# Performance work log

Measured on AMD Instinct MI355X. Metric: run time of the kernel, lower is better.

The kernel has to match this reference:

```python
import jax, jax.numpy as jnp
import numpy as np

N = 50000   # nodes
E = 640000  # edges (before self-loops)
D = 128     # in_channels = hidden_channels = out_channels
EPS_BN = 1e-5


def _gat(x, src, dst, W, a_src, a_dst, b, heads, concat):
    """PyG-style GATConv (self-loops already appended to src/dst)."""
    n = x.shape[0]
    C = W.shape[1] // heads
    xp = (x @ W).reshape(n, heads, C)                      # [N,H,C]
    asrc = jnp.sum(xp * a_src, -1)                          # [N,H]
    adst = jnp.sum(xp * a_dst, -1)                          # [N,H]
    e = jax.nn.leaky_relu(asrc[src] + adst[dst], 0.2)       # [Etot,H]
    m = jax.ops.segment_max(e, dst, num_segments=n)
    ex = jnp.exp(e - m[dst])
    s = jax.ops.segment_sum(ex, dst, num_segments=n)
    alpha = ex / (s[dst] + 1e-16)                           # segment softmax
    out = jax.ops.segment_sum(xp[src] * alpha[..., None], dst, num_segments=n)
    out = out.reshape(n, heads * C) if concat else out.mean(1)
    return out + b


def _gru(x, h, Wih, Whh, bih, bhh):
    gi = x @ Wih + bih
    gh = h @ Whh + bhh
    ir, iz, inn = jnp.split(gi, 3, -1)
    hr, hz, hn = jnp.split(gh, 3, -1)
    r = jax.nn.sigmoid(ir + hr)
    z = jax.nn.sigmoid(iz + hz)
    nn_ = jnp.tanh(inn + r * hn)
    return (1.0 - z) * nn_ + z * h


def setup_inputs() -> dict:
    key = jax.random.key(0)
    ks = jax.random.split(key, 32)
    f32 = jnp.float32
    p = lambda k, shape, s=0.1: jax.random.normal(k, shape, f32) * s
    inp = {
        "node_features": jax.random.normal(ks[0], (N, D), f32),
        "edge_index": jax.random.randint(ks[1], (2, E), 0, N),
        "x_prev1": jax.random.normal(ks[2], (N, D), f32),
        "x_prev2": jax.random.normal(ks[3], (N, D), f32),
        "ts": jax.random.uniform(ks[4], (N, 1), f32),
        # TimeEncode params
        "basis_freq": jnp.asarray(1.0 / 10 ** np.linspace(0, 9, D), f32),
        "phase": jnp.zeros((D,), f32),
        # MergeLayer: Linear(2D -> D)
        "merge_W": p(ks[5], (2 * D, D)),
        "merge_b": p(ks[6], (D,)),
        # layer1 GATConv(D -> D, heads=1, concat)
        "gat1_W": p(ks[7], (D, D)),
        "gat1_asrc": p(ks[8], (1, D)),
        "gat1_adst": p(ks[9], (1, D)),
        "gat1_b": p(ks[10], (D,)),
        # layer1 GRUCell(D, D)
        "gru1_Wih": p(ks[11], (D, 3 * D)),
        "gru1_Whh": p(ks[12], (D, 3 * D)),
        "gru1_bih": p(ks[13], (3 * D,)),
        "gru1_bhh": p(ks[14], (3 * D,)),
        # layer2 GATConv(D -> D, heads=1, concat=False)
        "gat2_W": p(ks[15], (D, D)),
        "gat2_asrc": p(ks[16], (1, D)),
        "gat2_adst": p(ks[17], (1, D)),
        "gat2_b": p(ks[18], (D,)),
        # layer2 GRUCell(D, D)
        "gru2_Wih": p(ks[19], (D, 3 * D)),
        "gru2_Whh": p(ks[20], (D, 3 * D)),
        "gru2_bih": p(ks[21], (3 * D,)),
        "gru2_bhh": p(ks[22], (3 * D,)),
        # skip connection Linear(D -> D)
        "skip_W": p(ks[23], (D, D)),
        "skip_b": p(ks[24], (D,)),
    }
    return inp


def reference(node_features, edge_index, x_prev1, x_prev2, ts,
              basis_freq, phase, merge_W, merge_b,
              gat1_W, gat1_asrc, gat1_adst, gat1_b,
              gru1_Wih, gru1_Whh, gru1_bih, gru1_bhh,
              gat2_W, gat2_asrc, gat2_adst, gat2_b,
              gru2_Wih, gru2_Whh, gru2_bih, gru2_bhh,
              skip_W, skip_b):
    n = node_features.shape[0]
    loop = jnp.arange(n)
    src = jnp.concatenate([edge_index[0], loop])  # add self-loops (PyG default)
    dst = jnp.concatenate([edge_index[1], loop])

    # TimeEncode: cos(ts * freq + phase) -> [N, D]
    t_embed = jnp.cos(ts * basis_freq[None, :] + phase[None, :])
    # MergeLayer
    x = jnp.concatenate([node_features, t_embed], -1) @ merge_W + merge_b

    # layer1: GAT + GRU, relu
    h1c = _gat(x, src, dst, gat1_W, gat1_asrc, gat1_adst, gat1_b, 1, True)
    H1 = jax.nn.relu(_gru(h1c, x_prev1, gru1_Wih, gru1_Whh, gru1_bih, gru1_bhh))

    # layer2: GAT + GRU + skip + fresh BatchNorm1d (training stats, identity affine)
    h2c = _gat(H1, src, dst, gat2_W, gat2_asrc, gat2_adst, gat2_b, 1, False)
    H2 = _gru(h2c, x_prev2, gru2_Wih, gru2_Whh, gru2_bih, gru2_bhh)
    H2 = H2 + (x @ skip_W + skip_b)
    mu = H2.mean(0)
    var = H2.var(0)
    H2 = (H2 - mu) / jnp.sqrt(var + EPS_BN)
    return (H1, H2)
```

## Files before the change

### kernel.cpp

```cpp
#include <hip/hip_runtime.h>
#include <math.h>

#define D 128
#define D3 384

typedef __attribute__((ext_vector_type(8))) short bf16x8;
typedef __attribute__((ext_vector_type(4))) float f32x4;
typedef __attribute__((ext_vector_type(4))) unsigned int u32x4;

__device__ __forceinline__ float fsigmoid(float x){
  return __builtin_amdgcn_rcpf(1.0f + __expf(-x));
}
__device__ __forceinline__ float ftanh(float x){
  float e = __expf(2.0f * x);
  return 1.0f - 2.0f * __builtin_amdgcn_rcpf(e + 1.0f);
}

__device__ __forceinline__ unsigned short f2bf(float f){
  unsigned u = __float_as_uint(f);
  return (unsigned short)((u + 0x7FFFu + ((u >> 16) & 1u)) >> 16);
}

__device__ __forceinline__ int slot16(int c, int row){ return (c + 2 * (row & 7)) & 15; }
__device__ __forceinline__ int slot32(int c, int row){ return (c + 2 * (row & 7)) & 31; }

__global__ __launch_bounds__(256) void k_init0(int* __restrict__ cnt, float* __restrict__ bns, int n){
  int idx = blockIdx.x * 256 + threadIdx.x;
  if (idx < n) cnt[idx] = 0;
  if (idx < 2 * D) bns[idx] = 0.0f;
}

__global__ __launch_bounds__(256) void k_wpackall(
    const float* __restrict__ mergeW, const float* __restrict__ g0, const float* __restrict__ g1,
    const float* __restrict__ sk, const float* __restrict__ ih0, const float* __restrict__ hh0,
    const float* __restrict__ ih1, const float* __restrict__ hh1,
    unsigned short* __restrict__ Pm, unsigned short* __restrict__ Pg0, unsigned short* __restrict__ Pg1,
    unsigned short* __restrict__ Psk, unsigned short* __restrict__ Pu0, unsigned short* __restrict__ Pu1){
  int idx = blockIdx.x * 256 + threadIdx.x;
  if (idx < 32768){
    int i = idx;
    int j = i & 7, l15 = (i >> 3) & 15, lg = (i >> 7) & 3, nf = (i >> 9) & 1, kk = (i >> 10) & 7, w = (i >> 13) & 3;
    int col = w * 32 + nf * 16 + l15, k = (kk * 4 + lg) * 8 + j;
    Pm[i] = f2bf(mergeW[k * 128 + col]);
  } else if (idx < 81920){
    int seg = (idx - 32768) >> 14;
    int i = (idx - 32768) & 16383;
    const float* W = seg == 0 ? g0 : (seg == 1 ? g1 : sk);
    unsigned short* P = seg == 0 ? Pg0 : (seg == 1 ? Pg1 : Psk);
    int j = i & 7, l15 = (i >> 3) & 15, lg = (i >> 7) & 3, nf = (i >> 9) & 1, kk = (i >> 10) & 3, w = (i >> 12) & 3;
    int col = w * 32 + nf * 16 + l15, k = (kk * 4 + lg) * 8 + j;
    P[i] = f2bf(W[k * 128 + col]);
  } else if (idx < 278528){
    int seg = (idx - 81920) / 98304;
    int i = (idx - 81920) % 98304;
    const float* Wih = seg ? ih1 : ih0;
    const float* Whh = seg ? hh1 : hh0;
    unsigned short* P = seg ? Pu1 : Pu0;
    int j = i & 7, l15 = (i >> 3) & 15, lg = (i >> 7) & 3;
    int r9 = i >> 9; int t = r9 % 6; int r = r9 / 6; int kk = r & 3, w = r >> 2;
    int col = (t >> 1) * 128 + w * 16 + l15, k = (kk * 4 + lg) * 8 + j;
    P[i] = f2bf((t & 1 ? Whh : Wih)[k * 384 + col]);
  }
}

__global__ __launch_bounds__(256) void k_merge(const float* __restrict__ nf, const float* __restrict__ ts,
                                               const float* __restrict__ freq, const float* __restrict__ phase,
                                               const unsigned short* __restrict__ Pm,
                                               const float* __restrict__ bias,
                                               unsigned short* __restrict__ xb, int M){
  __shared__ __align__(16) unsigned short Alds[64 * 256];
  const int tid = threadIdx.x;
  const int lane = tid & 63;
  const int w = tid >> 6;
  const int row0 = blockIdx.y * 64;

  #pragma unroll
  for (int r = 0; r < 8; ++r){
    int u = r * 256 + tid;
    int row = u >> 5, c16 = u & 31;
    int gr = row0 + row;
    union { unsigned short s[8]; bf16x8 v; } t;
    if (gr < M){
      if (c16 < 16){
        const float* p = nf + (size_t)gr * 128 + c16 * 8;
        float4 f0 = *(const float4*)p, f1 = *(const float4*)(p + 4);
        t.s[0]=f2bf(f0.x); t.s[1]=f2bf(f0.y); t.s[2]=f2bf(f0.z); t.s[3]=f2bf(f0.w);
        t.s[4]=f2bf(f1.x); t.s[5]=f2bf(f1.y); t.s[6]=f2bf(f1.z); t.s[7]=f2bf(f1.w);
      } else {
        float tv = ts[gr];
        int ch0 = (c16 - 16) * 8;
        float4 fq0 = *(const float4*)&freq[ch0],  fq1 = *(const float4*)&freq[ch0 + 4];
        float4 ph0 = *(const float4*)&phase[ch0], ph1 = *(const float4*)&phase[ch0 + 4];
        t.s[0]=f2bf(__cosf(tv*fq0.x+ph0.x)); t.s[1]=f2bf(__cosf(tv*fq0.y+ph0.y));
        t.s[2]=f2bf(__cosf(tv*fq0.z+ph0.z)); t.s[3]=f2bf(__cosf(tv*fq0.w+ph0.w));
        t.s[4]=f2bf(__cosf(tv*fq1.x+ph1.x)); t.s[5]=f2bf(__cosf(tv*fq1.y+ph1.y));
        t.s[6]=f2bf(__cosf(tv*fq1.z+ph1.z)); t.s[7]=f2bf(__cosf(tv*fq1.w+ph1.w));
      }
    } else {
      #pragma unroll
      for (int q = 0; q < 8; ++q) t.s[q] = 0;
    }
    *(bf16x8*)&Alds[row * 256 + slot32(c16, row) * 8] = t.v;
  }
  __syncthreads();

  f32x4 acc[4][2];
  #pragma unroll
  for (int mf = 0; mf < 4; ++mf)
    #pragma unroll
    for (int nfi = 0; nfi < 2; ++nfi)
      #pragma unroll
      for (int i = 0; i < 4; ++i) acc[mf][nfi][i] = 0.0f;

  const int l15 = lane & 15, lg = lane >> 4;
  #pragma unroll
  for (int kk = 0; kk < 8; ++kk){
    const int c16 = kk * 4 + lg;
    bf16x8 a[4], b[2];
    #pragma unroll
    for (int nfi = 0; nfi < 2; ++nfi)
      b[nfi] = *(const bf16x8*)&Pm[(size_t)((w * 8 + kk) * 2 + nfi) * 512 + lane * 8];
    #pragma unroll
    for (int mf = 0; mf < 4; ++mf){
      int row = mf * 16 + l15;
      a[mf] = *(bf16x8*)&Alds[row * 256 + slot32(c16, row) * 8];
    }
    #pragma unroll
    for (int mf = 0; mf < 4; ++mf)
      #pragma unroll
      for (int nfi = 0; nfi < 2; ++nfi)
        acc[mf][nfi] = __builtin_amdgcn_mfma_f32_16x16x32_bf16(a[mf], b[nfi], acc[mf][nfi], 0, 0, 0);
  }

  #pragma unroll
  for (int nfi = 0; nfi < 2; ++nfi){
    int c = w * 32 + nfi * 16 + l15;
    float bv = bias[c];
    #pragma unroll
    for (int mf = 0; mf < 4; ++mf)
      #pragma unroll
      for (int i = 0; i < 4; ++i){
        int rr = row0 + mf * 16 + lg * 4 + i;
        if (rr < M) xb[(size_t)rr * 128 + c] = f2bf(acc[mf][nfi][i] + bv);
      }
  }
}

template<bool ABF16, bool OUTBF, bool ACCUM, bool BIAS>
__global__ __launch_bounds__(256) void k_mgemm(const void* __restrict__ Av,
                                               const unsigned short* __restrict__ Pg,
                                               const float* __restrict__ bias,
                                               void* __restrict__ Cv, int M){
  __shared__ __align__(16) unsigned short Alds[64 * 128];
  const int tid = threadIdx.x;
  const int lane = tid & 63;
  const int w = tid >> 6;
  const int row0 = blockIdx.y * 64;

  #pragma unroll
  for (int r = 0; r < 4; ++r){
    int u = r * 256 + tid;
    int row = u >> 4, c16 = u & 15;
    int gr = row0 + row;
    int c16s = slot16(c16, row);
    if (ABF16){
      u32x4 v = {0,0,0,0};
      if (gr < M) v = *(const u32x4*)((const unsigned short*)Av + (size_t)gr * 128 + c16 * 8);
      *(u32x4*)&Alds[row * 128 + c16s * 8] = v;
    } else {
      float4 f0 = make_float4(0.f,0.f,0.f,0.f), f1 = f0;
      if (gr < M){
        const float* p = (const float*)Av + (size_t)gr * 128 + c16 * 8;
        f0 = *(const float4*)p; f1 = *(const float4*)(p + 4);
      }
      union { unsigned short s[8]; bf16x8 v; } t;
      t.s[0]=f2bf(f0.x); t.s[1]=f2bf(f0.y); t.s[2]=f2bf(f0.z); t.s[3]=f2bf(f0.w);
      t.s[4]=f2bf(f1.x); t.s[5]=f2bf(f1.y); t.s[6]=f2bf(f1.z); t.s[7]=f2bf(f1.w);
      *(bf16x8*)&Alds[row * 128 + c16s * 8] = t.v;
    }
  }
  __syncthreads();

  f32x4 acc[4][2];
  #pragma unroll
  for (int mf = 0; mf < 4; ++mf)
    #pragma unroll
    for (int nfi = 0; nfi < 2; ++nfi)
      #pragma unroll
      for (int i = 0; i < 4; ++i) acc[mf][nfi][i] = 0.0f;

  const int l15 = lane & 15, lg = lane >> 4;
  #pragma unroll
  for (int kk = 0; kk < 4; ++kk){
    const int c16 = kk * 4 + lg;
    bf16x8 a[4], b[2];
    #pragma unroll
    for (int nfi = 0; nfi < 2; ++nfi)
      b[nfi] = *(const bf16x8*)&Pg[(size_t)((w * 4 + kk) * 2 + nfi) * 512 + lane * 8];
    #pragma unroll
    for (int mf = 0; mf < 4; ++mf){
      int row = mf * 16 + l15;
      a[mf] = *(bf16x8*)&Alds[row * 128 + slot16(c16, row) * 8];
    }
    #pragma unroll
    for (int mf = 0; mf < 4; ++mf)
      #pragma unroll
      for (int nfi = 0; nfi < 2; ++nfi)
        acc[mf][nfi] = __builtin_amdgcn_mfma_f32_16x16x32_bf16(a[mf], b[nfi], acc[mf][nfi], 0, 0, 0);
  }

  #pragma unroll
  for (int nfi = 0; nfi < 2; ++nfi){
    int c = w * 32 + nfi * 16 + l15;
    float bv = BIAS ? bias[c] : 0.0f;
    #pragma unroll
    for (int mf = 0; mf < 4; ++mf)
      #pragma unroll
      for (int i = 0; i < 4; ++i){
        int rr = row0 + mf * 16 + lg * 4 + i;
        if (rr < M){
          size_t o = (size_t)rr * 128 + c;
          float v = acc[mf][nfi][i] + bv;
          if (OUTBF){
            ((unsigned short*)Cv)[o] = f2bf(v);
          } else {
            float* C = (float*)Cv;
            if (ACCUM) v += C[o];
            C[o] = v;
          }
        }
      }
  }
}

__global__ __launch_bounds__(256) void k_attn(const unsigned short* __restrict__ xpb,
                                              const float* __restrict__ a_s, const float* __restrict__ a_d,
                                              float* __restrict__ asrc, float* __restrict__ adst, int n){
  int wave = (blockIdx.x * 256 + threadIdx.x) >> 6;
  int lane = threadIdx.x & 63;
  if (wave >= n) return;
  unsigned u = *(const unsigned*)&xpb[(size_t)wave * D + 2 * lane];
  float lo = __uint_as_float(u << 16);
  float hi = __uint_as_float(u & 0xFFFF0000u);
  float2 as2 = *(const float2*)&a_s[2 * lane];
  float2 ad2 = *(const float2*)&a_d[2 * lane];
  float sa = lo * as2.x + hi * as2.y;
  float sd = lo * ad2.x + hi * ad2.y;
  #pragma unroll
  for (int off = 32; off > 0; off >>= 1){
    sa += __shfl_down(sa, off);
    sd += __shfl_down(sd, off);
  }
  if (lane == 0){ asrc[wave] = sa; adst[wave] = sd; }
}

__global__ __launch_bounds__(256) void k_hist(const int* __restrict__ ei, int* __restrict__ cnt, int e, int etot){
  int t = blockIdx.x * 256 + threadIdx.x;
  if (t >= etot) return;
  int d_ = (t < e) ? ei[e + t] : (t - e);
  atomicAdd(&cnt[d_], 1);
}

__global__ __launch_bounds__(256) void k_scan1(const int* __restrict__ cnt, int* __restrict__ off,
                                               int* __restrict__ bsum, int n){
  __shared__ int sm[256];
  int i = blockIdx.x * 256 + threadIdx.x;
  int v = (i < n) ? cnt[i] : 0;
  sm[threadIdx.x] = v;
  __syncthreads();
  #pragma unroll
  for (int d = 1; d < 256; d <<= 1){
    int t = (threadIdx.x >= d) ? sm[threadIdx.x - d] : 0;
    __syncthreads();
    sm[threadIdx.x] += t;
    __syncthreads();
  }
  if (i < n) off[i] = sm[threadIdx.x] - v;
  if (threadIdx.x == 255) bsum[blockIdx.x] = sm[255];
}

__global__ __launch_bounds__(256) void k_scan2(int* __restrict__ bsum, int nb){
  __shared__ int sm[256];
  int v = (threadIdx.x < nb) ? bsum[threadIdx.x] : 0;
  sm[threadIdx.x] = v;
  __syncthreads();
  #pragma unroll
  for (int d = 1; d < 256; d <<= 1){
    int t = (threadIdx.x >= d) ? sm[threadIdx.x - d] : 0;
    __syncthreads();
    sm[threadIdx.x] += t;
    __syncthreads();
  }
  if (threadIdx.x < nb) bsum[threadIdx.x] = sm[threadIdx.x] - v;
}

__global__ __launch_bounds__(256) void k_scan3(int* __restrict__ off, const int* __restrict__ bsum,
                                               int* __restrict__ cursor, int n, int etot){
  int i = blockIdx.x * 256 + threadIdx.x;
  if (i < n){
    int o = off[i] + bsum[blockIdx.x];
    off[i] = o;
    cursor[i] = o;
  }
  if (i == 0) off[n] = etot;
}

__global__ __launch_bounds__(256) void k_scatter(const int* __restrict__ ei, int* __restrict__ cursor,
                                                 int* __restrict__ csr, int e, int etot){
  int t = blockIdx.x * 256 + threadIdx.x;
  if (t >= etot) return;
  int s_, d_;
  if (t < e){ s_ = ei[t]; d_ = ei[e + t]; } else { s_ = d_ = t - e; }
  int pos = atomicAdd(&cursor[d_], 1);
  csr[pos] = s_;
}

__global__ __launch_bounds__(256) void k_gatconv(const int* __restrict__ off, const int* __restrict__ csr,
                                                 const float* __restrict__ asrc, const float* __restrict__ adst,
                                                 const unsigned short* __restrict__ xpb,
                                                 const float* __restrict__ bias,
                                                 unsigned short* __restrict__ outb, int n){
  int w = (blockIdx.x * 256 + threadIdx.x) >> 6;
  int lane = threadIdx.x & 63;
  if (w >= n) return;
  const int o0 = off[w], o1 = off[w + 1];
  const float ad = adst[w];
  float m = -1e30f;
  for (int j = o0 + lane; j < o1; j += 64){
    float v = asrc[csr[j]] + ad;
    v = (v > 0.0f) ? v : 0.2f * v;
    m = fmaxf(m, v);
  }
  #pragma unroll
  for (int d = 32; d > 0; d >>= 1) m = fmaxf(m, __shfl_xor(m, d));
  float s = 0.0f, acc0 = 0.0f, acc1 = 0.0f;
  for (int base = o0; base < o1; base += 64){
    int j = base + lane;
    float wgt = 0.0f;
    int src = 0;
    if (j < o1){
      src = csr[j];
      float v = asrc[src] + ad;
      v = (v > 0.0f) ? v : 0.2f * v;
      wgt = __expf(v - m);
    }
    s += wgt;
    const int cnt8 = (min(64, o1 - base) + 7) & ~7;
    const int wbits = __float_as_int(wgt);
    for (int t = 0; t < cnt8; t += 8){
      unsigned uu[8]; float wq[8];
      #pragma unroll
      for (int q = 0; q < 8; ++q){
        int sr = __builtin_amdgcn_readlane(src, t + q);
        wq[q] = __int_as_float(__builtin_amdgcn_readlane(wbits, t + q));
        uu[q] = *(const unsigned*)&xpb[(size_t)sr * D + 2 * lane];
      }
      #pragma unroll
      for (int q = 0; q < 8; ++q){
        acc0 = fmaf(wq[q], __uint_as_float(uu[q] << 16), acc0);
        acc1 = fmaf(wq[q], __uint_as_float(uu[q] & 0xFFFF0000u), acc1);
      }
    }
  }
  #pragma unroll
  for (int d = 32; d > 0; d >>= 1) s += __shfl_xor(s, d);
  float inv = 1.0f / (s + 1e-16f);
  float2 bv = *(const float2*)&bias[2 * lane];
  unsigned pack = ((unsigned)f2bf(acc1 * inv + bv.y) << 16) | f2bf(acc0 * inv + bv.x);
  *(unsigned*)&outb[(size_t)w * D + 2 * lane] = pack;
}

template<int RELU>
__global__ __launch_bounds__(512) void k_grugemm(const unsigned short* __restrict__ hgb,
                                                 const float* __restrict__ xprev,
                                                 const unsigned short* __restrict__ Pu,
                                                 const float* __restrict__ bih,
                                                 const float* __restrict__ bhh,
                                                 float* __restrict__ out, int n){
  __shared__ __align__(16) unsigned short A1lds[64 * 128];
  __shared__ __align__(16) unsigned short A2lds[64 * 128];
  const int tid = threadIdx.x;
  const int lane = tid & 63;
  const int w = tid >> 6;
  const int row0 = blockIdx.x * 64;

  #pragma unroll
  for (int r = 0; r < 2; ++r){
    int u = r * 512 + tid;
    int row = u >> 4, c16 = u & 15;
    int gr = row0 + row;
    int c16s = slot16(c16, row);
    u32x4 v1 = {0,0,0,0};
    union { unsigned short s[8]; bf16x8 v; } t2;
    #pragma unroll
    for (int q = 0; q < 8; ++q) t2.s[q] = 0;
    if (gr < n){
      v1 = *(const u32x4*)(hgb + (size_t)gr * 128 + c16 * 8);
      const float* p = xprev + (size_t)gr * 128 + c16 * 8;
      float4 f0 = *(const float4*)p, f1 = *(const float4*)(p + 4);
      t2.s[0]=f2bf(f0.x); t2.s[1]=f2bf(f0.y); t2.s[2]=f2bf(f0.z); t2.s[3]=f2bf(f0.w);
      t2.s[4]=f2bf(f1.x); t2.s[5]=f2bf(f1.y); t2.s[6]=f2bf(f1.z); t2.s[7]=f2bf(f1.w);
    }
    *(u32x4*)&A1lds[row * 128 + c16s * 8] = v1;
    *(bf16x8*)&A2lds[row * 128 + c16s * 8] = t2.v;
  }
  __syncthreads();

  f32x4 accR[4], accZ[4], accN[4], accH[4];
  #pragma unroll
  for (int mf = 0; mf < 4; ++mf)
    #pragma unroll
    for (int i = 0; i < 4; ++i){ accR[mf][i]=0.f; accZ[mf][i]=0.f; accN[mf][i]=0.f; accH[mf][i]=0.f; }

  const int l15 = lane & 15, lg = lane >> 4;
  const int cw = w * 16 + l15;
  #pragma unroll
  for (int kk = 0; kk < 4; ++kk){
    const int c16 = kk * 4 + lg;
    const unsigned short* Pb = Pu + (size_t)(w * 4 + kk) * 3072 + lane * 8;
    bf16x8 bir = *(const bf16x8*)&Pb[0];
    bf16x8 bhr = *(const bf16x8*)&Pb[512];
    bf16x8 biz = *(const bf16x8*)&Pb[1024];
    bf16x8 bhz = *(const bf16x8*)&Pb[1536];
    bf16x8 bin = *(const bf16x8*)&Pb[2048];
    bf16x8 bhn = *(const bf16x8*)&Pb[2560];
    bf16x8 a1[4], a2[4];
    #pragma unroll
    for (int mf = 0; mf < 4; ++mf){
      int row = mf * 16 + l15;
      int o = row * 128 + slot16(c16, row) * 8;
      a1[mf] = *(bf16x8*)&A1lds[o];
      a2[mf] = *(bf16x8*)&A2lds[o];
    }
    #pragma unroll
    for (int mf = 0; mf < 4; ++mf){
      accR[mf] = __builtin_amdgcn_mfma_f32_16x16x32_bf16(a1[mf], bir, accR[mf], 0, 0, 0);
      accR[mf] = __builtin_amdgcn_mfma_f32_16x16x32_bf16(a2[mf], bhr, accR[mf], 0, 0, 0);
      accZ[mf] = __builtin_amdgcn_mfma_f32_16x16x32_bf16(a1[mf], biz, accZ[mf], 0, 0, 0);
      accZ[mf] = __builtin_amdgcn_mfma_f32_16x16x32_bf16(a2[mf], bhz, accZ[mf], 0, 0, 0);
      accN[mf] = __builtin_amdgcn_mfma_f32_16x16x32_bf16(a1[mf], bin, accN[mf], 0, 0, 0);
      accH[mf] = __builtin_amdgcn_mfma_f32_16x16x32_bf16(a2[mf], bhn, accH[mf], 0, 0, 0);
    }
  }

  const float sbR = bih[cw] + bhh[cw];
  const float sbZ = bih[cw + 128] + bhh[cw + 128];
  const float biN = bih[cw + 256], bhN = bhh[cw + 256];
  #pragma unroll
  for (int mf = 0; mf < 4; ++mf)
    #pragma unroll
    for (int i = 0; i < 4; ++i){
      int rr = row0 + mf * 16 + lg * 4 + i;
      if (rr < n){
        float r  = fsigmoid(accR[mf][i] + sbR);
        float z  = fsigmoid(accZ[mf][i] + sbZ);
        float nn = ftanh(accN[mf][i] + biN + r * (accH[mf][i] + bhN));
        float hp = xprev[(size_t)rr * 128 + cw];
        float h = (1.0f - z) * nn + z * hp;
        if (RELU) h = fmaxf(h, 0.0f);
        out[(size_t)rr * 128 + cw] = h;
      }
    }
}

__global__ __launch_bounds__(256) void k_bnreduce(const float* __restrict__ H, float* __restrict__ bns, int n){
  int c = threadIdx.x & 127;
  int half = threadIdx.x >> 7;
  int r0 = blockIdx.x * 128;
  int rend = min(r0 + 128, n);
  float s0 = 0.0f, s1 = 0.0f;
  for (int r = r0 + half; r < rend; r += 2){
    float v = H[(size_t)r * D + c];
    s0 += v; s1 += v * v;
  }
  __shared__ float sm[2][128];
  if (half){ sm[0][c] = s0; sm[1][c] = s1; }
  __syncthreads();
  if (!half){
    s0 += sm[0][c]; s1 += sm[1][c];
    atomicAdd(&bns[c], s0);
    atomicAdd(&bns[D + c], s1);
  }
}

__global__ __launch_bounds__(256) void k_bnnorm(float* __restrict__ H, const float* __restrict__ bns, int n){
  int idx = blockIdx.x * 256 + threadIdx.x;
  if (idx >= n * D) return;
  int c = idx & 127;
  float inv_n = 1.0f / (float)n;
  float mu = bns[c] * inv_n;
  float var = bns[D + c] * inv_n - mu * mu;
  H[idx] = (H[idx] - mu) / sqrtf(var + 1e-5f);
}

extern "C" void kernel_launch(void* const* d_in, const int* in_sizes, int n_in,
                              void* d_out, int out_size, void* d_ws, size_t ws_size,
                              hipStream_t stream){
  const float* nf     = (const float*)d_in[0];
  const int*   ei     = (const int*)  d_in[1];
  const float* xprev[2] = { (const float*)d_in[2], (const float*)d_in[3] };
  const float* ts     = (const float*)d_in[4];
  const float* freq   = (const float*)d_in[5];
  const float* phase  = (const float*)d_in[6];
  const float* mergeW = (const float*)d_in[7];
  const float* mergeb = (const float*)d_in[8];
  const float* gatW[2]  = { (const float*)d_in[9],  (const float*)d_in[17] };
  const float* gatAS[2] = { (const float*)d_in[10], (const float*)d_in[18] };
  const float* gatAD[2] = { (const float*)d_in[11], (const float*)d_in[19] };
  const float* gatB[2]  = { (const float*)d_in[12], (const float*)d_in[20] };
  const float* Wih[2]   = { (const float*)d_in[13], (const float*)d_in[21] };
  const float* Whh[2]   = { (const float*)d_in[14], (const float*)d_in[22] };
  const float* bih[2]   = { (const float*)d_in[15], (const float*)d_in[23] };
  const float* bhh[2]   = { (const float*)d_in[16], (const float*)d_in[24] };
  const float* skipW  = (const float*)d_in[25];
  const float* skipb  = (const float*)d_in[26];

  const int n = in_sizes[0] / D;
  const int e = in_sizes[1] / 2;
  const int etot = e + n;
  const size_t nd = (size_t)n * D;

  float* ws   = (float*)d_ws;
  float* asrc = ws;
  float* adst = asrc + n;
  float* bns  = adst + n;
  int*   off  = (int*)(bns + 2 * D);
  int*   cnt  = off + n + 1;
  int*   bsum = cnt + n;
  int*   csr  = bsum + 256;
  uintptr_t pa = ((uintptr_t)(csr + etot) + 15) & ~(uintptr_t)15;
  unsigned short* Pm  = (unsigned short*)pa;
  unsigned short* Pg0 = Pm  + 32768;
  unsigned short* Pg1 = Pg0 + 16384;
  unsigned short* Psk = Pg1 + 16384;
  unsigned short* Pu0 = Psk + 16384;
  unsigned short* Pu1 = Pu0 + 98304;
  unsigned short* xb  = Pu1 + 98304;
  unsigned short* xpb = xb  + nd;
  unsigned short* hgb = xpb + nd;

  float* H1 = (float*)d_out;
  float* H2 = H1 + nd;

  const dim3 b256(256);
  const int nb_nd = (int)((nd + 255) / 256);
  const int nb_e  = (etot + 255) / 256;
  const int nb_n  = (n + 255) / 256;
  const int grows = (n + 63) / 64;
  const dim3 gm1(1, grows);
  const int gru_blocks = (n + 63) / 64;
  const int nb_wave = (int)(((size_t)n * 64 + 255) / 256);

  k_init0<<<nb_n, b256, 0, stream>>>(cnt, bns, n);
  k_hist<<<nb_e, b256, 0, stream>>>(ei, cnt, e, etot);
  k_scan1<<<nb_n, b256, 0, stream>>>(cnt, off, bsum, n);
  k_scan2<<<1, b256, 0, stream>>>(bsum, nb_n);
  k_scan3<<<nb_n, b256, 0, stream>>>(off, bsum, cnt, n, etot);
  k_scatter<<<nb_e, b256, 0, stream>>>(ei, cnt, csr, e, etot);

  k_wpackall<<<(278528 + 255) / 256, b256, 0, stream>>>(
      mergeW, gatW[0], gatW[1], skipW, Wih[0], Whh[0], Wih[1], Whh[1],
      Pm, Pg0, Pg1, Psk, Pu0, Pu1);

  k_merge<<<gm1, b256, 0, stream>>>(nf, ts, freq, phase, Pm, mergeb, xb, n);

  for (int L = 0; L < 2; ++L){
    float* gout = (L == 0) ? H1 : H2;
    const unsigned short* wtg = (L == 0) ? Pg0 : Pg1;
    const unsigned short* pu  = (L == 0) ? Pu0 : Pu1;
    if (L == 0)
      k_mgemm<true , true, false, false><<<gm1, b256, 0, stream>>>(xb, wtg, nullptr, xpb, n);
    else
      k_mgemm<false, true, false, false><<<gm1, b256, 0, stream>>>(H1, wtg, nullptr, xpb, n);
    k_attn<<<nb_wave, b256, 0, stream>>>(xpb, gatAS[L], gatAD[L], asrc, adst, n);
    k_gatconv<<<nb_wave, b256, 0, stream>>>(off, csr, asrc, adst, xpb, gatB[L], hgb, n);
    if (L == 0)
      k_grugemm<1><<<gru_blocks, dim3(512), 0, stream>>>(hgb, xprev[0], pu, bih[0], bhh[0], gout, n);
    else
      k_grugemm<0><<<gru_blocks, dim3(512), 0, stream>>>(hgb, xprev[1], pu, bih[1], bhh[1], gout, n);
  }

  k_mgemm<true, false, true, true><<<gm1, b256, 0, stream>>>(xb, Psk, skipb, H2, n);
  k_bnreduce<<<(n + 127) / 128, b256, 0, stream>>>(H2, bns, n);
  k_bnnorm<<<nb_nd, b256, 0, stream>>>(H2, bns, n);
}
```

Baseline: 461.7 us.

## Fuse attention and BN reductions into GEMM epilogues; bucket edges for CSR build

```diff
diff --git a/kernel.cpp b/kernel.cpp
--- a/kernel.cpp
+++ b/kernel.cpp
@@ -24,10 +24,12 @@
 __device__ __forceinline__ int slot16(int c, int row){ return (c + 2 * (row & 7)) & 15; }
 __device__ __forceinline__ int slot32(int c, int row){ return (c + 2 * (row & 7)) & 31; }
 
-__global__ __launch_bounds__(256) void k_init0(int* __restrict__ cnt, float* __restrict__ bns, int n){
+__global__ __launch_bounds__(256) void k_init0(int* __restrict__ cnt, float* __restrict__ bns,
+                                               int* __restrict__ gbh, int n){
   int idx = blockIdx.x * 256 + threadIdx.x;
   if (idx < n) cnt[idx] = 0;
   if (idx < 2 * D) bns[idx] = 0.0f;
+  if (idx < 256) gbh[idx] = 0;
 }
 
 __global__ __launch_bounds__(256) void k_wpackall(
@@ -146,16 +148,27 @@
   }
 }
 
-template<bool ABF16, bool OUTBF, bool ACCUM, bool BIAS>
+template<bool ABF16, bool OUTBF, bool ACCUM, bool BIAS, bool ATTN, bool BNRED>
 __global__ __launch_bounds__(256) void k_mgemm(const void* __restrict__ Av,
                                                const unsigned short* __restrict__ Pg,
                                                const float* __restrict__ bias,
-                                               void* __restrict__ Cv, int M){
+                                               void* __restrict__ Cv, int M,
+                                               const float* __restrict__ a_s, const float* __restrict__ a_d,
+                                               float* __restrict__ asrc, float* __restrict__ adst,
+                                               float* __restrict__ bns){
   __shared__ __align__(16) unsigned short Alds[64 * 128];
+  __shared__ float attS[64], attD[64];
+  __shared__ float bn2[256];
   const int tid = threadIdx.x;
   const int lane = tid & 63;
   const int w = tid >> 6;
   const int row0 = blockIdx.y * 64;
+
+  if (ATTN){
+    if (tid < 64) attS[tid] = 0.0f;
+    else if (tid < 128) attD[tid - 64] = 0.0f;
+  }
+  if (BNRED) bn2[tid] = 0.0f;
 
   #pragma unroll
   for (int r = 0; r < 4; ++r){
@@ -209,10 +222,19 @@
         acc[mf][nfi] = __builtin_amdgcn_mfma_f32_16x16x32_bf16(a[mf], b[nfi], acc[mf][nfi], 0, 0, 0);
   }
 
+  const int c0 = w * 32 + l15;
+  const int c1 = c0 + 16;
+  float as0, as1, ad0, ad1;
+  if (ATTN){
+    as0 = a_s[c0]; as1 = a_s[c1];
+    ad0 = a_d[c0]; ad1 = a_d[c1];
+  }
+
   #pragma unroll
   for (int nfi = 0; nfi < 2; ++nfi){
     int c = w * 32 + nfi * 16 + l15;
     float bv = BIAS ? bias[c] : 0.0f;
+    float bs = 0.0f, bq = 0.0f;
     #pragma unroll
     for (int mf = 0; mf < 4; ++mf)
       #pragma unroll
@@ -228,37 +250,50 @@
             if (ACCUM) v += C[o];
             C[o] = v;
           }
+          if (BNRED){ bs += v; bq += v * v; }
         }
       }
-  }
-}
-
-__global__ __launch_bounds__(256) void k_attn(const unsigned short* __restrict__ xpb,
-                                              const float* __restrict__ a_s, const float* __restrict__ a_d,
-                                              float* __restrict__ asrc, float* __restrict__ adst, int n){
-  int wave = (blockIdx.x * 256 + threadIdx.x) >> 6;
-  int lane = threadIdx.x & 63;
-  if (wave >= n) return;
-  unsigned u = *(const unsigned*)&xpb[(size_t)wave * D + 2 * lane];
-  float lo = __uint_as_float(u << 16);
-  float hi = __uint_as_float(u & 0xFFFF0000u);
-  float2 as2 = *(const float2*)&a_s[2 * lane];
-  float2 ad2 = *(const float2*)&a_d[2 * lane];
-  float sa = lo * as2.x + hi * as2.y;
-  float sd = lo * ad2.x + hi * ad2.y;
-  #pragma unroll
-  for (int off = 32; off > 0; off >>= 1){
-    sa += __shfl_down(sa, off);
-    sd += __shfl_down(sd, off);
-  }
-  if (lane == 0){ asrc[wave] = sa; adst[wave] = sd; }
-}
-
-__global__ __launch_bounds__(256) void k_hist(const int* __restrict__ ei, int* __restrict__ cnt, int e, int etot){
-  int t = blockIdx.x * 256 + threadIdx.x;
-  if (t >= etot) return;
-  int d_ = (t < e) ? ei[e + t] : (t - e);
-  atomicAdd(&cnt[d_], 1);
+    if (BNRED){
+      atomicAdd(&bn2[c], bs);
+      atomicAdd(&bn2[128 + c], bq);
+    }
+  }
+
+  if (ATTN){
+    #pragma unroll
+    for (int mf = 0; mf < 4; ++mf)
+      #pragma unroll
+      for (int i = 0; i < 4; ++i){
+        int row = mf * 16 + lg * 4 + i;
+        atomicAdd(&attS[row], acc[mf][0][i] * as0 + acc[mf][1][i] * as1);
+        atomicAdd(&attD[row], acc[mf][0][i] * ad0 + acc[mf][1][i] * ad1);
+      }
+    __syncthreads();
+    if (tid < 64 && row0 + tid < M){
+      asrc[row0 + tid] = attS[tid];
+      adst[row0 + tid] = attD[tid];
+    }
+  }
+  if (BNRED){
+    __syncthreads();
+    atomicAdd(&bns[tid], bn2[tid]);
+  }
+}
+
+__global__ __launch_bounds__(256) void k_hist(const int* __restrict__ ei, int* __restrict__ cnt,
+                                              int* __restrict__ gbh, int e, int etot){
+  __shared__ int bh[256];
+  bh[threadIdx.x] = 0;
+  __syncthreads();
+  int i0 = blockIdx.x * 4096;
+  int iend = min(i0 + 4096, etot);
+  for (int t = i0 + threadIdx.x; t < iend; t += 256){
+    int d_ = (t < e) ? ei[e + t] : (t - e);
+    atomicAdd(&cnt[d_], 1);
+    atomicAdd(&bh[d_ >> 8], 1);
+  }
+  __syncthreads();
+  if (bh[threadIdx.x]) atomicAdd(&gbh[threadIdx.x], bh[threadIdx.x]);
 }
 
 __global__ __launch_bounds__(256) void k_scan1(const int* __restrict__ cnt, int* __restrict__ off,
@@ -279,7 +314,8 @@
   if (threadIdx.x == 255) bsum[blockIdx.x] = sm[255];
 }
 
-__global__ __launch_bounds__(256) void k_scan2(int* __restrict__ bsum, int nb){
+__global__ __launch_bounds__(256) void k_scan2(int* __restrict__ bsum, int nb,
+                                               const int* __restrict__ gbh, int* __restrict__ gbc){
   __shared__ int sm[256];
   int v = (threadIdx.x < nb) ? bsum[threadIdx.x] : 0;
   sm[threadIdx.x] = v;
@@ -292,6 +328,18 @@
     __syncthreads();
   }
   if (threadIdx.x < nb) bsum[threadIdx.x] = sm[threadIdx.x] - v;
+  __syncthreads();
+  int v2 = gbh[threadIdx.x];
+  sm[threadIdx.x] = v2;
+  __syncthreads();
+  #pragma unroll
+  for (int d = 1; d < 256; d <<= 1){
+    int t = (threadIdx.x >= d) ? sm[threadIdx.x - d] : 0;
+    __syncthreads();
+    sm[threadIdx.x] += t;
+    __syncthreads();
+  }
+  gbc[threadIdx.x] = sm[threadIdx.x] - v2;
 }
 
 __global__ __launch_bounds__(256) void k_scan3(int* __restrict__ off, const int* __restrict__ bsum,
@@ -305,14 +353,39 @@
   if (i == 0) off[n] = etot;
 }
 
-__global__ __launch_bounds__(256) void k_scatter(const int* __restrict__ ei, int* __restrict__ cursor,
-                                                 int* __restrict__ csr, int e, int etot){
+__global__ __launch_bounds__(256) void k_bucket1(const int* __restrict__ ei, int* __restrict__ gbc,
+                                                 uint2* __restrict__ ebuck, int e, int etot){
+  __shared__ int h[256], base[256], lc[256];
+  const int tid = threadIdx.x;
+  h[tid] = 0;
+  __syncthreads();
+  int i0 = blockIdx.x * 1024;
+  int iend = min(i0 + 1024, etot);
+  uint2 ed[4]; int ne = 0;
+  for (int t = i0 + tid; t < iend; t += 256){
+    int s_, d_;
+    if (t < e){ s_ = ei[t]; d_ = ei[e + t]; } else { s_ = d_ = t - e; }
+    ed[ne].x = (unsigned)s_; ed[ne].y = (unsigned)d_; ++ne;
+    atomicAdd(&h[d_ >> 8], 1);
+  }
+  __syncthreads();
+  base[tid] = h[tid] ? atomicAdd(&gbc[tid], h[tid]) : 0;
+  lc[tid] = 0;
+  __syncthreads();
+  for (int q = 0; q < ne; ++q){
+    int b = ed[q].y >> 8;
+    int p = base[b] + atomicAdd(&lc[b], 1);
+    ebuck[p] = ed[q];
+  }
+}
+
+__global__ __launch_bounds__(256) void k_bucket2(const uint2* __restrict__ ebuck, int* __restrict__ cursor,
+                                                 int* __restrict__ csr, int etot){
   int t = blockIdx.x * 256 + threadIdx.x;
   if (t >= etot) return;
-  int s_, d_;
-  if (t < e){ s_ = ei[t]; d_ = ei[e + t]; } else { s_ = d_ = t - e; }
-  int pos = atomicAdd(&cursor[d_], 1);
-  csr[pos] = s_;
+  uint2 p = ebuck[t];
+  int pos = atomicAdd(&cursor[p.y], 1);
+  csr[pos] = (int)p.x;
 }
 
 __global__ __launch_bounds__(256) void k_gatconv(const int* __restrict__ off, const int* __restrict__ csr,
@@ -461,26 +534,6 @@
         out[(size_t)rr * 128 + cw] = h;
       }
     }
-}
-
-__global__ __launch_bounds__(256) void k_bnreduce(const float* __restrict__ H, float* __restrict__ bns, int n){
-  int c = threadIdx.x & 127;
-  int half = threadIdx.x >> 7;
-  int r0 = blockIdx.x * 128;
-  int rend = min(r0 + 128, n);
-  float s0 = 0.0f, s1 = 0.0f;
-  for (int r = r0 + half; r < rend; r += 2){
-    float v = H[(size_t)r * D + c];
-    s0 += v; s1 += v * v;
-  }
-  __shared__ float sm[2][128];
-  if (half){ sm[0][c] = s0; sm[1][c] = s1; }
-  __syncthreads();
-  if (!half){
-    s0 += sm[0][c]; s1 += sm[1][c];
-    atomicAdd(&bns[c], s0);
-    atomicAdd(&bns[D + c], s1);
-  }
 }
 
 __global__ __launch_bounds__(256) void k_bnnorm(float* __restrict__ H, const float* __restrict__ bns, int n){
@@ -527,8 +580,12 @@
   int*   off  = (int*)(bns + 2 * D);
   int*   cnt  = off + n + 1;
   int*   bsum = cnt + n;
-  int*   csr  = bsum + 256;
-  uintptr_t pa = ((uintptr_t)(csr + etot) + 15) & ~(uintptr_t)15;
+  int*   gbh  = bsum + 256;
+  int*   gbc  = gbh + 256;
+  int*   csr  = gbc + 256;
+  uintptr_t ba = ((uintptr_t)(csr + etot) + 7) & ~(uintptr_t)7;
+  uint2* ebuck = (uint2*)ba;
+  uintptr_t pa = ((uintptr_t)(ebuck + etot) + 15) & ~(uintptr_t)15;
   unsigned short* Pm  = (unsigned short*)pa;
   unsigned short* Pg0 = Pm  + 32768;
   unsigned short* Pg1 = Pg0 + 16384;
@@ -551,12 +608,13 @@
   const int gru_blocks = (n + 63) / 64;
   const int nb_wave = (int)(((size_t)n * 64 + 255) / 256);
 
-  k_init0<<<nb_n, b256, 0, stream>>>(cnt, bns, n);
-  k_hist<<<nb_e, b256, 0, stream>>>(ei, cnt, e, etot);
+  k_init0<<<nb_n, b256, 0, stream>>>(cnt, bns, gbh, n);
+  k_hist<<<(etot + 4095) / 4096, b256, 0, stream>>>(ei, cnt, gbh, e, etot);
   k_scan1<<<nb_n, b256, 0, stream>>>(cnt, off, bsum, n);
-  k_scan2<<<1, b256, 0, stream>>>(bsum, nb_n);
+  k_scan2<<<1, b256, 0, stream>>>(bsum, nb_n, gbh, gbc);
   k_scan3<<<nb_n, b256, 0, stream>>>(off, bsum, cnt, n, etot);
-  k_scatter<<<nb_e, b256, 0, stream>>>(ei, cnt, csr, e, etot);
+  k_bucket1<<<(etot + 1023) / 1024, b256, 0, stream>>>(ei, gbc, ebuck, e, etot);
+  k_bucket2<<<nb_e, b256, 0, stream>>>(ebuck, cnt, csr, etot);
 
   k_wpackall<<<(278528 + 255) / 256, b256, 0, stream>>>(
       mergeW, gatW[0], gatW[1], skipW, Wih[0], Whh[0], Wih[1], Whh[1],
@@ -569,10 +627,11 @@
     const unsigned short* wtg = (L == 0) ? Pg0 : Pg1;
     const unsigned short* pu  = (L == 0) ? Pu0 : Pu1;
     if (L == 0)
-      k_mgemm<true , true, false, false><<<gm1, b256, 0, stream>>>(xb, wtg, nullptr, xpb, n);
+      k_mgemm<true , true, false, false, true, false><<<gm1, b256, 0, stream>>>(
+          xb, wtg, nullptr, xpb, n, gatAS[0], gatAD[0], asrc, adst, nullptr);
     else
-      k_mgemm<false, true, false, false><<<gm1, b256, 0, stream>>>(H1, wtg, nullptr, xpb, n);
-    k_attn<<<nb_wave, b256, 0, stream>>>(xpb, gatAS[L], gatAD[L], asrc, adst, n);
+      k_mgemm<false, true, false, false, true, false><<<gm1, b256, 0, stream>>>(
+          H1, wtg, nullptr, xpb, n, gatAS[1], gatAD[1], asrc, adst, nullptr);
     k_gatconv<<<nb_wave, b256, 0, stream>>>(off, csr, asrc, adst, xpb, gatB[L], hgb, n);
     if (L == 0)
       k_grugemm<1><<<gru_blocks, dim3(512), 0, stream>>>(hgb, xprev[0], pu, bih[0], bhh[0], gout, n);
@@ -580,7 +639,7 @@
       k_grugemm<0><<<gru_blocks, dim3(512), 0, stream>>>(hgb, xprev[1], pu, bih[1], bhh[1], gout, n);
   }
 
-  k_mgemm<true, false, true, true><<<gm1, b256, 0, stream>>>(xb, Psk, skipb, H2, n);
-  k_bnreduce<<<(n + 127) / 128, b256, 0, stream>>>(H2, bns, n);
+  k_mgemm<true, false, true, true, false, true><<<gm1, b256, 0, stream>>>(
+      xb, Psk, skipb, H2, n, nullptr, nullptr, nullptr, nullptr, bns);
   k_bnnorm<<<nb_nd, b256, 0, stream>>>(H2, bns, n);
 }
```

Measured after the change: 546.4 us. +18.3%, slower.
